# Optimization experiments

Measured on AMD Instinct MI355X. Metric: run time of the kernel, lower is better.

## Reference

```python
import jax, jax.numpy as jnp
import numpy as np
import math

SCALE = 35.0
MARGIN = 0.5
THRESH = -math.cos(MARGIN)          # easy_margin=False branch
SIN_M = math.sin(MARGIN)
OUT_INDICATOR = 1.0                 # easy_margin=False branch

B, D, C = 256, 128, 100000


def setup_inputs() -> dict:
    key = jax.random.key(0)
    k1, k2, k3 = jax.random.split(key, 3)
    feat = jax.random.normal(k1, (B, D), dtype=jnp.float32)
    # xavier_uniform over [class_num, feature_dim]
    limit = math.sqrt(6.0 / (C + D))
    weights = jax.random.uniform(k2, (C, D), dtype=jnp.float32, minval=-limit, maxval=limit)
    label = jax.random.randint(k3, (B,), 0, C, dtype=jnp.int64)
    return {"feat": feat, "weights": weights, "label": label}


def reference(feat, weights, label):
    # cosine similarity between l2-normalized features and class weights
    nf = feat / jnp.linalg.norm(feat, axis=-1, keepdims=True)          # [B, D]
    nw = weights / jnp.linalg.norm(weights, axis=-1, keepdims=True)    # [C, D]
    cos = jnp.einsum('bd,cd->bc', nf, nw)                              # [B, C]
    innerproduct_logits = jnp.einsum('bd,cd->bc', feat, weights)       # [B, C]

    rows = jnp.arange(cos.shape[0])
    cos_gt = cos[rows, label]                                          # [B]

    # margin tables are zero off the ground-truth column, so
    # cos(acos(cos)+0) == cos there: only the gt entry changes.
    cond = cos_gt > THRESH
    add_m = jnp.where(cond, MARGIN, 0.0)
    ext = jnp.where(cond, 0.0, -MARGIN * SIN_M) * OUT_INDICATOR
    # clip for acos numerical safety (matmul of normalized vecs can exceed 1 by eps)
    gt_marg = jnp.cos(jnp.arccos(jnp.clip(cos_gt, -1.0, 1.0)) + add_m) + ext

    marginal_logits = (SCALE * cos).at[rows, label].set(SCALE * gt_marg)
    return (cos, marginal_logits, innerproduct_logits)
```

## Files before the change

### kernel.cpp

```cpp
#include <hip/hip_runtime.h>
#include <math.h>

using short8  = __attribute__((ext_vector_type(8))) short;
using floatx4 = __attribute__((ext_vector_type(4))) float;

namespace {
constexpr int   kB      = 256;
constexpr int   kD      = 128;
constexpr int   kC      = 100000;
constexpr float kScale  = 35.0f;
constexpr float kCosM   = 0.87758256189037276f;
constexpr float kSinM   = 0.47942553860420301f;
constexpr float kThresh = -0.87758256189037276f;
constexpr float kExt    = -0.5f * 0.47942553860420301f;

constexpr size_t kWgtBfOff  = 0;
constexpr size_t kFeatBfOff = (size_t)kC * 256;
constexpr size_t kRwOff     = kFeatBfOff + (size_t)kB * 256;
constexpr size_t kRfOff     = kRwOff + (size_t)kC * 4;
}

__device__ inline unsigned short f2bf(float f) {
    unsigned u = __builtin_bit_cast(unsigned, f);
    return (unsigned short)((u + 0x7fffu + ((u >> 16) & 1u)) >> 16);
}

__device__ inline void async16(void* lds, const void* g) {
    __builtin_amdgcn_global_load_lds(
        (const __attribute__((address_space(1))) void*)g,
        (__attribute__((address_space(3))) void*)lds, 16, 0, 0);
}

__global__ __launch_bounds__(256)
void arcface_prep(const float* __restrict__ feat,
                  const float* __restrict__ wgt,
                  unsigned char* __restrict__ ws) {
    const int wid = blockIdx.x * 4 + (threadIdx.x >> 6);
    const int l   = threadIdx.x & 63;
    if (wid >= kC + kB) return;
    const bool isW = wid < kC;
    const float* src = isW ? (wgt + (size_t)wid * kD)
                           : (feat + (size_t)(wid - kC) * kD);
    const float2 v = *(const float2*)(src + 2 * l);
    float s = v.x * v.x + v.y * v.y;
    #pragma unroll
    for (int off = 32; off > 0; off >>= 1) s += __shfl_down(s, off, 64);

    const unsigned packed = (unsigned)f2bf(v.x) | ((unsigned)f2bf(v.y) << 16);
    if (isW) {
        unsigned* row = (unsigned*)(ws + kWgtBfOff + (size_t)wid * 256);
        row[(l + (wid & 15) * 4) & 63] = packed;
        if (l == 0) *(float*)(ws + kRwOff + (size_t)wid * 4) = rsqrtf(s);
    } else {
        unsigned* row = (unsigned*)(ws + kFeatBfOff + (size_t)(wid - kC) * 256);
        row[l] = packed;
        if (l == 0) *(float*)(ws + kRfOff + (size_t)(wid - kC) * 4) = rsqrtf(s);
    }
}

__global__ __launch_bounds__(256, 2)
void arcface_gemm(const unsigned char* __restrict__ ws,
                  float* __restrict__ out_cos,
                  float* __restrict__ out_marg,
                  float* __restrict__ out_ip) {
    __shared__ short sB[2][64 * 128];
    __shared__ float sScr[4][16 * 68];

    const int t   = threadIdx.x;
    const int l   = t & 63;
    const int w   = t >> 6;
    const int q   = l >> 4;
    const int c16 = l & 15;
    const int m0  = w * 64;

    const short* featbf = (const short*)(ws + kFeatBfOff);
    const short* wgtbf  = (const short*)(ws + kWgtBfOff);
    const float* rw_g   = (const float*)(ws + kRwOff);
    const float* rf_g   = (const float*)(ws + kRfOff);

    const int tile0 = blockIdx.x * 2;

    #pragma unroll
    for (int it = 0; it < 2; ++it) {
        const char* src = (const char*)wgtbf + (size_t)(tile0 + it) * 16384;
        char* dst = (char*)&sB[it][0];
        #pragma unroll
        for (int p = 0; p < 4; ++p)
            async16(dst + p * 4096 + t * 16, src + p * 4096 + t * 16);
    }

    short8 aF[4][4];
    #pragma unroll
    for (int mi = 0; mi < 4; ++mi)
        #pragma unroll
        for (int kq = 0; kq < 4; ++kq)
            aF[mi][kq] = *(const short8*)(featbf + (size_t)(m0 + mi * 16 + c16) * kD + kq * 32 + q * 8);

    __syncthreads();

    #pragma unroll
    for (int it = 0; it < 2; ++it) {
        const short* bbuf = &sB[it][0];
        floatx4 acc[4][4];
        #pragma unroll
        for (int mi = 0; mi < 4; ++mi)
            #pragma unroll
            for (int nt = 0; nt < 4; ++nt)
                acc[mi][nt] = (floatx4){0.f, 0.f, 0.f, 0.f};

        #pragma unroll
        for (int kq = 0; kq < 4; ++kq) {
            short8 bF[4];
            const int s = (q + c16 + kq * 4) & 15;
            #pragma unroll
            for (int nt = 0; nt < 4; ++nt)
                bF[nt] = *(const short8*)(bbuf + (nt * 16 + c16) * 128 + s * 8);
            #pragma unroll
            for (int mi = 0; mi < 4; ++mi)
                #pragma unroll
                for (int nt = 0; nt < 4; ++nt)
                    acc[mi][nt] = __builtin_amdgcn_mfma_f32_16x16x32_bf16(
                        aF[mi][kq], bF[nt], acc[mi][nt], 0, 0, 0);
        }

        const int c0n = (tile0 + it) * 64;
        float* scr = &sScr[w][0];
        #pragma unroll
        for (int mi = 0; mi < 4; ++mi) {
            #pragma unroll
            for (int nt = 0; nt < 4; ++nt)
                #pragma unroll
                for (int r = 0; r < 4; ++r)
                    scr[(q * 4 + r) * 68 + nt * 16 + c16] = acc[mi][nt][r];
            #pragma unroll
            for (int jj = 0; jj < 4; ++jj) {
                const int rr = q + 4 * jj;
                const floatx4 ip = *(const floatx4*)(scr + rr * 68 + c16 * 4);
                const int m = m0 + mi * 16 + rr;
                const int c = c0n + c16 * 4;
                if (c < kC) {
                    const float rf = rf_g[m];
                    const floatx4 rw4 = *(const floatx4*)(rw_g + c);
                    const floatx4 cs = ip * rf * rw4;
                    const size_t o = (size_t)m * kC + c;
                    *(floatx4*)(out_ip + o)   = ip;
                    *(floatx4*)(out_cos + o)  = cs;
                    *(floatx4*)(out_marg + o) = cs * kScale;
                }
            }
        }
    }
}

__global__ void arcface_fixup(const int* __restrict__ label,
                              const float* __restrict__ out_cos,
                              float* __restrict__ out_marg) {
    const int b = threadIdx.x;
    bool is64 = true;
    #pragma unroll
    for (int i = 1; i < 24; i += 2) is64 = is64 && (label[i] == 0);
    const int c = is64 ? label[2 * b] : label[b];
    const size_t idx = (size_t)b * kC + c;
    const float cosv = out_cos[idx];
    const float cc = fminf(1.f, fmaxf(-1.f, cosv));
    float marg;
    if (cosv > kThresh) {
        marg = cc * kCosM - sqrtf(fmaxf(0.f, 1.f - cc * cc)) * kSinM;
    } else {
        marg = cc + kExt;
    }
    out_marg[idx] = kScale * marg;
}

extern "C" void kernel_launch(void* const* d_in, const int* in_sizes, int n_in,
                              void* d_out, int out_size, void* d_ws, size_t ws_size,
                              hipStream_t stream) {
    const float* feat  = (const float*)d_in[0];
    const float* wgt   = (const float*)d_in[1];
    const int*   label = (const int*)d_in[2];
    float* out_cos  = (float*)d_out;
    float* out_marg = out_cos  + (size_t)kB * kC;
    float* out_ip   = out_marg + (size_t)kB * kC;
    unsigned char* ws = (unsigned char*)d_ws;

    arcface_prep<<<(kC + kB + 3) / 4, 256, 0, stream>>>(feat, wgt, ws);
    arcface_gemm<<<782, 256, 0, stream>>>(ws, out_cos, out_marg, out_ip);
    arcface_fixup<<<1, 256, 0, stream>>>(label, out_cos, out_marg);
}
```

Before: 369.2 us.

## Fuse weight bf16 conversion and norm computation into the GEMM kernel

The prep kernel no longer converts the 100000x128 weight matrix to bf16 or computes its inverse norms. The GEMM kernel now loads fp32 weights straight into swizzled LDS, computes row norms and bf16 fragments on the fly, and processes one 64-column tile per block instead of two. Output stores become nontemporal. This drops a full write and read of the weight workspace, at the cost of doubling LDS traffic for fp32 weights and adding conversion ALU work inside the GEMM.

```diff
diff --git a/kernel.cpp b/kernel.cpp
--- a/kernel.cpp
+++ b/kernel.cpp
@@ -14,10 +14,8 @@
 constexpr float kThresh = -0.87758256189037276f;
 constexpr float kExt    = -0.5f * 0.47942553860420301f;
 
-constexpr size_t kWgtBfOff  = 0;
-constexpr size_t kFeatBfOff = (size_t)kC * 256;
-constexpr size_t kRwOff     = kFeatBfOff + (size_t)kB * 256;
-constexpr size_t kRfOff     = kRwOff + (size_t)kC * 4;
+constexpr size_t kFeatBfOff = 0;
+constexpr size_t kRfOff     = (size_t)kB * 256;
 }
 
 __device__ inline unsigned short f2bf(float f) {
@@ -32,39 +30,27 @@
 }
 
 __global__ __launch_bounds__(256)
-void arcface_prep(const float* __restrict__ feat,
-                  const float* __restrict__ wgt,
-                  unsigned char* __restrict__ ws) {
+void arcface_prep(const float* __restrict__ feat, unsigned char* __restrict__ ws) {
     const int wid = blockIdx.x * 4 + (threadIdx.x >> 6);
     const int l   = threadIdx.x & 63;
-    if (wid >= kC + kB) return;
-    const bool isW = wid < kC;
-    const float* src = isW ? (wgt + (size_t)wid * kD)
-                           : (feat + (size_t)(wid - kC) * kD);
-    const float2 v = *(const float2*)(src + 2 * l);
+    const float2 v = *(const float2*)(feat + (size_t)wid * kD + 2 * l);
     float s = v.x * v.x + v.y * v.y;
     #pragma unroll
     for (int off = 32; off > 0; off >>= 1) s += __shfl_down(s, off, 64);
-
     const unsigned packed = (unsigned)f2bf(v.x) | ((unsigned)f2bf(v.y) << 16);
-    if (isW) {
-        unsigned* row = (unsigned*)(ws + kWgtBfOff + (size_t)wid * 256);
-        row[(l + (wid & 15) * 4) & 63] = packed;
-        if (l == 0) *(float*)(ws + kRwOff + (size_t)wid * 4) = rsqrtf(s);
-    } else {
-        unsigned* row = (unsigned*)(ws + kFeatBfOff + (size_t)(wid - kC) * 256);
-        row[l] = packed;
-        if (l == 0) *(float*)(ws + kRfOff + (size_t)(wid - kC) * 4) = rsqrtf(s);
-    }
+    ((unsigned*)(ws + kFeatBfOff + (size_t)wid * 256))[l] = packed;
+    if (l == 0) *(float*)(ws + kRfOff + (size_t)wid * 4) = rsqrtf(s);
 }
 
 __global__ __launch_bounds__(256, 2)
-void arcface_gemm(const unsigned char* __restrict__ ws,
+void arcface_gemm(const float* __restrict__ wgt,
+                  const unsigned char* __restrict__ ws,
                   float* __restrict__ out_cos,
                   float* __restrict__ out_marg,
                   float* __restrict__ out_ip) {
-    __shared__ short sB[2][64 * 128];
+    __shared__ float sW[64 * 128];
     __shared__ float sScr[4][16 * 68];
+    __shared__ float sRw[64];
 
     const int t   = threadIdx.x;
     const int l   = t & 63;
@@ -72,22 +58,20 @@
     const int q   = l >> 4;
     const int c16 = l & 15;
     const int m0  = w * 64;
+    const int c0  = blockIdx.x * 64;
+
+    #pragma unroll
+    for (int p = 0; p < 8; ++p) {
+        const int o    = p * 4096 + t * 16;
+        const int row  = o >> 9;
+        const int col  = o & 511;
+        const int swz  = ((row & 15) << 5) | ((row & 4) << 2);
+        const int srow = min(c0 + row, kC - 1);
+        async16((char*)sW + o, (const char*)wgt + (size_t)srow * 512 + (col ^ swz));
+    }
 
     const short* featbf = (const short*)(ws + kFeatBfOff);
-    const short* wgtbf  = (const short*)(ws + kWgtBfOff);
-    const float* rw_g   = (const float*)(ws + kRwOff);
     const float* rf_g   = (const float*)(ws + kRfOff);
-
-    const int tile0 = blockIdx.x * 2;
-
-    #pragma unroll
-    for (int it = 0; it < 2; ++it) {
-        const char* src = (const char*)wgtbf + (size_t)(tile0 + it) * 16384;
-        char* dst = (char*)&sB[it][0];
-        #pragma unroll
-        for (int p = 0; p < 4; ++p)
-            async16(dst + p * 4096 + t * 16, src + p * 4096 + t * 16);
-    }
 
     short8 aF[4][4];
     #pragma unroll
@@ -98,55 +82,74 @@
 
     __syncthreads();
 
+    floatx4 acc[4][4];
     #pragma unroll
-    for (int it = 0; it < 2; ++it) {
-        const short* bbuf = &sB[it][0];
-        floatx4 acc[4][4];
+    for (int mi = 0; mi < 4; ++mi)
+        #pragma unroll
+        for (int nt = 0; nt < 4; ++nt)
+            acc[mi][nt] = (floatx4){0.f, 0.f, 0.f, 0.f};
+
+    float s2[4] = {0.f, 0.f, 0.f, 0.f};
+
+    #pragma unroll
+    for (int kq = 0; kq < 4; ++kq) {
+        short8 bF[4];
+        #pragma unroll
+        for (int nt = 0; nt < 4; ++nt) {
+            const int row = nt * 16 + c16;
+            const int swz = ((row & 15) << 5) | ((row & 4) << 2);
+            const int cb  = kq * 128 + q * 32;
+            const floatx4 w0 = *(const floatx4*)((const char*)sW + row * 512 + ((cb)      ^ swz));
+            const floatx4 w1 = *(const floatx4*)((const char*)sW + row * 512 + ((cb + 16) ^ swz));
+            s2[nt] += w0[0]*w0[0] + w0[1]*w0[1] + w0[2]*w0[2] + w0[3]*w0[3]
+                    + w1[0]*w1[0] + w1[1]*w1[1] + w1[2]*w1[2] + w1[3]*w1[3];
+            short8 b;
+            b[0] = (short)f2bf(w0[0]); b[1] = (short)f2bf(w0[1]);
+            b[2] = (short)f2bf(w0[2]); b[3] = (short)f2bf(w0[3]);
+            b[4] = (short)f2bf(w1[0]); b[5] = (short)f2bf(w1[1]);
+            b[6] = (short)f2bf(w1[2]); b[7] = (short)f2bf(w1[3]);
+            bF[nt] = b;
+        }
         #pragma unroll
         for (int mi = 0; mi < 4; ++mi)
             #pragma unroll
             for (int nt = 0; nt < 4; ++nt)
-                acc[mi][nt] = (floatx4){0.f, 0.f, 0.f, 0.f};
+                acc[mi][nt] = __builtin_amdgcn_mfma_f32_16x16x32_bf16(
+                    aF[mi][kq], bF[nt], acc[mi][nt], 0, 0, 0);
+    }
 
+    #pragma unroll
+    for (int nt = 0; nt < 4; ++nt) {
+        float s = s2[nt];
+        s += __shfl_xor(s, 16, 64);
+        s += __shfl_xor(s, 32, 64);
+        sRw[nt * 16 + c16] = rsqrtf(s);
+    }
+
+    float* scr = &sScr[w][0];
+    const int  c   = c0 + c16 * 4;
+    const bool cok = c < kC;
+    const floatx4 rw4 = *(const floatx4*)(sRw + c16 * 4);
+
+    #pragma unroll
+    for (int mi = 0; mi < 4; ++mi) {
         #pragma unroll
-        for (int kq = 0; kq < 4; ++kq) {
-            short8 bF[4];
-            const int s = (q + c16 + kq * 4) & 15;
+        for (int nt = 0; nt < 4; ++nt)
             #pragma unroll
-            for (int nt = 0; nt < 4; ++nt)
-                bF[nt] = *(const short8*)(bbuf + (nt * 16 + c16) * 128 + s * 8);
-            #pragma unroll
-            for (int mi = 0; mi < 4; ++mi)
-                #pragma unroll
-                for (int nt = 0; nt < 4; ++nt)
-                    acc[mi][nt] = __builtin_amdgcn_mfma_f32_16x16x32_bf16(
-                        aF[mi][kq], bF[nt], acc[mi][nt], 0, 0, 0);
-        }
-
-        const int c0n = (tile0 + it) * 64;
-        float* scr = &sScr[w][0];
+            for (int r = 0; r < 4; ++r)
+                scr[(q * 4 + r) * 68 + nt * 16 + c16] = acc[mi][nt][r];
         #pragma unroll
-        for (int mi = 0; mi < 4; ++mi) {
-            #pragma unroll
-            for (int nt = 0; nt < 4; ++nt)
-                #pragma unroll
-                for (int r = 0; r < 4; ++r)
-                    scr[(q * 4 + r) * 68 + nt * 16 + c16] = acc[mi][nt][r];
-            #pragma unroll
-            for (int jj = 0; jj < 4; ++jj) {
-                const int rr = q + 4 * jj;
-                const floatx4 ip = *(const floatx4*)(scr + rr * 68 + c16 * 4);
-                const int m = m0 + mi * 16 + rr;
-                const int c = c0n + c16 * 4;
-                if (c < kC) {
-                    const float rf = rf_g[m];
-                    const floatx4 rw4 = *(const floatx4*)(rw_g + c);
-                    const floatx4 cs = ip * rf * rw4;
-                    const size_t o = (size_t)m * kC + c;
-                    *(floatx4*)(out_ip + o)   = ip;
-                    *(floatx4*)(out_cos + o)  = cs;
-                    *(floatx4*)(out_marg + o) = cs * kScale;
-                }
+        for (int jj = 0; jj < 4; ++jj) {
+            const int rr = q + 4 * jj;
+            const floatx4 ip = *(const floatx4*)(scr + rr * 68 + c16 * 4);
+            const int m = m0 + mi * 16 + rr;
+            if (cok) {
+                const float rf = rf_g[m];
+                const floatx4 cs = ip * rf * rw4;
+                const size_t o = (size_t)m * kC + c;
+                __builtin_nontemporal_store(ip,           (floatx4*)(out_ip + o));
+                __builtin_nontemporal_store(cs,           (floatx4*)(out_cos + o));
+                __builtin_nontemporal_store(cs * kScale,  (floatx4*)(out_marg + o));
             }
         }
     }
@@ -183,7 +186,7 @@
     float* out_ip   = out_marg + (size_t)kB * kC;
     unsigned char* ws = (unsigned char*)d_ws;
 
-    arcface_prep<<<(kC + kB + 3) / 4, 256, 0, stream>>>(feat, wgt, ws);
-    arcface_gemm<<<782, 256, 0, stream>>>(ws, out_cos, out_marg, out_ip);
+    arcface_prep<<<64, 256, 0, stream>>>(feat, ws);
+    arcface_gemm<<<(kC + 63) / 64, 256, 0, stream>>>(wgt, ws, out_cos, out_marg, out_ip);
     arcface_fixup<<<1, 256, 0, stream>>>(label, out_cos, out_marg);
 }
```

New measurement: 358.2 us. 1.03x faster.
